# Kernel tuning notes

Measured on AMD Instinct MI355X. Metric: run time of the kernel, lower is better.

## Reference

```python
import jax, jax.numpy as jnp
import numpy as np

N = 262144          # anchors
NUM_CLASSES = 80
DET_DIM = 4 + NUM_CLASSES
TOP_K = 1000
MAX_BOXES = 300
NMS_THRESHOLD = 0.4


def setup_inputs() -> dict:
    key = jax.random.key(0)
    k1, k2, k3, k4, k5 = jax.random.split(key, 5)
    # boxes in (x1, y1, x2, y2) format with x2 > x1, y2 > y1
    xy1 = jax.random.uniform(k1, (1, N, 2), dtype=jnp.float32) * 1000.0
    wh = jax.random.uniform(k2, (1, N, 2), dtype=jnp.float32) * 100.0 + 1.0
    boxes = jnp.concatenate([xy1, xy1 + wh], axis=-1)              # [1, N, 4]
    classification = jax.random.uniform(k3, (1, N, NUM_CLASSES), dtype=jnp.float32)
    detections = jax.random.normal(k4, (1, N, DET_DIM), dtype=jnp.float32)
    return {"boxes": boxes, "classification": classification, "detections": detections}


def _iou_matrix(b):
    # b: [K, 4] in (x1, y1, x2, y2)
    x1, y1, x2, y2 = b[:, 0], b[:, 1], b[:, 2], b[:, 3]
    area = (x2 - x1) * (y2 - y1)
    ix1 = jnp.maximum(x1[:, None], x1[None, :])
    iy1 = jnp.maximum(y1[:, None], y1[None, :])
    ix2 = jnp.minimum(x2[:, None], x2[None, :])
    iy2 = jnp.minimum(y2[:, None], y2[None, :])
    inter = jnp.maximum(ix2 - ix1, 0.0) * jnp.maximum(iy2 - iy1, 0.0)
    union = area[:, None] + area[None, :] - inter
    return inter / jnp.maximum(union, 1e-8)


def _nms(boxes, scores, iou_threshold, max_output_size):
    # Greedy NMS (tf.image.non_max_suppression semantics) on K boxes.
    K = boxes.shape[0]
    order = jnp.argsort(-scores)              # descending score
    iou = _iou_matrix(boxes[order])           # [K, K] in sorted order
    ar = jnp.arange(K)

    def body(suppressed, i):
        active = jnp.logical_not(suppressed[i])
        suppressed = suppressed | (active & (iou[i] > iou_threshold) & (ar > i))
        return suppressed, active

    _, keep = jax.lax.scan(body, jnp.zeros((K,), jnp.bool_), ar)
    # fixed-size selection of kept positions (in score order), padded with K
    sel = jnp.nonzero(keep, size=max_output_size, fill_value=K)[0]
    valid = sel < K
    order_pad = jnp.concatenate([order, jnp.zeros((1,), order.dtype)])
    return order_pad[sel], valid


def reference(boxes, classification, detections):
    b = boxes[0]                               # [N, 4]
    c = classification[0]                      # [N, C]
    d = detections[0]                          # [N, D]
    scores = jnp.max(c, axis=1)                # per-anchor best class score
    scores_k, idx_k = jax.lax.top_k(scores, TOP_K)
    b_k = b[idx_k]                             # [TOP_K, 4]
    d_k = d[idx_k]                             # [TOP_K, D]
    nms_idx, valid = _nms(b_k, scores_k, NMS_THRESHOLD, MAX_BOXES)
    # original returns a ragged [1, n_kept, D]; we return fixed [1, MAX_BOXES, D]
    # with invalid rows zeroed (padding for jit-compatibility)
    out = d_k[nms_idx] * valid[:, None].astype(d_k.dtype)
    return out[None]                           # [1, MAX_BOXES, D]
```

## Files before the change

### kernel.cpp

```cpp
#include <hip/hip_runtime.h>
#include <stdint.h>

#define N_ANCH 262144
#define NUM_CLASSES 80
#define DET_DIM 84
#define TOP_K 1000
#define MAX_BOXES 300
#define NMS_THR 0.4f

#define OFF_KEYS   0u
#define OFF_HIST1  (N_ANCH * 4u)
#define OFF_HIST2  (OFF_HIST1 + 16384u)
#define OFF_HIST3  (OFF_HIST2 + 16384u)
#define OFF_STATE  (OFF_HIST3 + 1024u)
#define OFF_LISTA  (OFF_STATE + 64u)
#define OFF_LISTB  (OFF_LISTA + 4096u)
#define OFF_TOPK   (OFF_LISTB + 16384u)
#define OFF_BOXK   (OFF_TOPK + 4096u)
#define OFF_MASK   (OFF_BOXK + 16384u)
#define OFF_SEL    (OFF_MASK + 131072u)

#define ZERO_WORDS ((16384u + 16384u + 1024u + 64u) / 4u)

__global__ __launch_bounds__(256) void k_init(uint32_t* __restrict__ z) {
    uint32_t tid = blockIdx.x * 256u + threadIdx.x;
    if (tid < ZERO_WORDS) z[tid] = 0u;
}

__global__ __launch_bounds__(256) void k_scores(const float* __restrict__ cls,
                                                uint32_t* __restrict__ keys,
                                                uint32_t* __restrict__ ghist1) {
    __shared__ uint32_t h[4096];
    for (int i = threadIdx.x; i < 4096; i += 256) h[i] = 0u;
    __syncthreads();
    int stride = gridDim.x * 256;
    for (int a = blockIdx.x * 256 + threadIdx.x; a < N_ANCH; a += stride) {
        const float4* q = (const float4*)(cls + (size_t)a * NUM_CLASSES);
        float m = -1.0f;
#pragma unroll
        for (int t = 0; t < 20; ++t) {
            float4 v = q[t];
            m = fmaxf(m, fmaxf(fmaxf(v.x, v.y), fmaxf(v.z, v.w)));
        }
        uint32_t key = __float_as_uint(m);
        keys[a] = key;
        atomicAdd(&h[key >> 20], 1u);
    }
    __syncthreads();
    for (int i = threadIdx.x; i < 4096; i += 256) {
        uint32_t v = h[i];
        if (v) atomicAdd(&ghist1[i], v);
    }
}

__device__ __forceinline__ void wave_scan_hist(const uint32_t* __restrict__ hist,
                                               int nbins, uint32_t k,
                                               uint32_t* __restrict__ out, int lane) {
    int per = nbins >> 6;
    int base = lane * per;
    uint32_t partial = 0;
    for (int b = 0; b < per; ++b) partial += hist[base + b];
    uint32_t si = partial;
#pragma unroll
    for (int off = 1; off < 64; off <<= 1) {
        uint32_t v = __shfl_down(si, off);
        if (lane + off < 64) si += v;
    }
    uint32_t se = si - partial;
    if (se < k && k <= si) {
        uint32_t running = se;
        for (int b = base + per - 1; b >= base; --b) {
            uint32_t hv = hist[b];
            running += hv;
            if (running >= k) {
                out[0] = (uint32_t)b;
                out[1] = k - (running - hv);
                break;
            }
        }
    }
}

__global__ __launch_bounds__(256) void k_pass2(const uint32_t* __restrict__ keys,
                                               const uint32_t* __restrict__ ghist1,
                                               uint32_t* __restrict__ ghist2,
                                               uint32_t* __restrict__ state) {
    __shared__ uint32_t sd[2];
    __shared__ uint32_t h[4096];
    if (threadIdx.x < 64) wave_scan_hist(ghist1, 4096, TOP_K, sd, threadIdx.x);
    for (int i = threadIdx.x; i < 4096; i += 256) h[i] = 0u;
    __syncthreads();
    uint32_t d1 = sd[0], k1 = sd[1];
    if (threadIdx.x == 0 && blockIdx.x == 0) { state[0] = d1; state[1] = k1; }
    int stride = gridDim.x * 256;
    for (int a = blockIdx.x * 256 + threadIdx.x; a < N_ANCH; a += stride) {
        uint32_t key = keys[a];
        if ((key >> 20) == d1) atomicAdd(&h[(key >> 8) & 0xFFFu], 1u);
    }
    __syncthreads();
    for (int i = threadIdx.x; i < 4096; i += 256) {
        uint32_t v = h[i];
        if (v) atomicAdd(&ghist2[i], v);
    }
}

__global__ __launch_bounds__(256) void k_pass3(const uint32_t* __restrict__ keys,
                                               const uint32_t* __restrict__ ghist2,
                                               uint32_t* __restrict__ ghist3,
                                               uint32_t* __restrict__ state) {
    __shared__ uint32_t sd[2];
    if (threadIdx.x < 64) {
        uint32_t k1 = state[1];
        wave_scan_hist(ghist2, 4096, k1, sd, threadIdx.x);
    }
    __syncthreads();
    uint32_t pre24 = (state[0] << 12) | sd[0];
    uint32_t k2 = sd[1];
    if (threadIdx.x == 0 && blockIdx.x == 0) { state[2] = pre24; state[3] = k2; }
    int stride = gridDim.x * 256;
    for (int a = blockIdx.x * 256 + threadIdx.x; a < N_ANCH; a += stride) {
        uint32_t key = keys[a];
        if ((key >> 8) == pre24) atomicAdd(&ghist3[key & 0xFFu], 1u);
    }
}

__global__ __launch_bounds__(256) void k_compact(const uint32_t* __restrict__ keys,
                                                 const uint32_t* __restrict__ ghist3,
                                                 uint32_t* __restrict__ state,
                                                 uint32_t* __restrict__ listA,
                                                 uint32_t* __restrict__ listB) {
    __shared__ uint32_t sd[2];
    if (threadIdx.x < 64) {
        uint32_t k2 = state[3];
        wave_scan_hist(ghist3, 256, k2, sd, threadIdx.x);
    }
    __syncthreads();
    uint32_t T = (state[2] << 8) | sd[0];
    if (threadIdx.x == 0 && blockIdx.x == 0) { state[4] = T; state[5] = sd[1]; }
    int stride = gridDim.x * 256;
    for (int a = blockIdx.x * 256 + threadIdx.x; a < N_ANCH; a += stride) {
        uint32_t key = keys[a];
        if (key > T) {
            uint32_t p = atomicAdd(&state[6], 1u);
            if (p < 1024u) listA[p] = (uint32_t)a;
        } else if (key == T) {
            uint32_t p = atomicAdd(&state[7], 1u);
            if (p < 4096u) listB[p] = (uint32_t)a;
        }
    }
}

__global__ __launch_bounds__(1024) void k_finalize(const uint32_t* __restrict__ keys,
                                                   const uint32_t* __restrict__ state,
                                                   const uint32_t* __restrict__ listA,
                                                   const uint32_t* __restrict__ listB,
                                                   uint32_t* __restrict__ topk,
                                                   const float4* __restrict__ boxes,
                                                   float4* __restrict__ boxk) {
    __shared__ unsigned long long A[1024];
    __shared__ uint32_t Bv[4096];
    __shared__ uint32_t tk[1000];
    int t = threadIdx.x;
    uint32_t cntA = state[6]; if (cntA > 999u) cntA = 999u;
    uint32_t cntB = state[7]; if (cntB > 4096u) cntB = 4096u;
    uint32_t r = TOP_K - cntA;

    unsigned long long wv = ~0ull;
    if (t < (int)cntA) {
        uint32_t idx = listA[t];
        uint32_t key = keys[idx];
        wv = ((unsigned long long)(key ^ 0xFFFFFFFFu) << 32) | (unsigned long long)idx;
    }
    A[t] = wv;
    __syncthreads();
    unsigned n2 = 1; while (n2 < cntA) n2 <<= 1;
    for (unsigned k = 2; k <= n2; k <<= 1) {
        for (unsigned j = k >> 1; j > 0; j >>= 1) {
            unsigned i = (unsigned)t;
            unsigned ixj = i ^ j;
            if (i < n2 && ixj > i) {
                unsigned long long a = A[i], b = A[ixj];
                bool up = ((i & k) == 0);
                if (up ? (a > b) : (a < b)) { A[i] = b; A[ixj] = a; }
            }
            __syncthreads();
        }
    }
    if (t < (int)cntA) tk[t] = (uint32_t)(A[t] & 0xFFFFFFFFull);

    unsigned n2b = 1; while (n2b < cntB) n2b <<= 1;
    for (unsigned i = (unsigned)t; i < n2b; i += 1024) Bv[i] = (i < cntB) ? listB[i] : 0xFFFFFFFFu;
    __syncthreads();
    for (unsigned k = 2; k <= n2b; k <<= 1) {
        for (unsigned j = k >> 1; j > 0; j >>= 1) {
            for (unsigned i = (unsigned)t; i < n2b; i += 1024) {
                unsigned ixj = i ^ j;
                if (ixj > i) {
                    uint32_t a = Bv[i], b = Bv[ixj];
                    bool up = ((i & k) == 0);
                    if (up ? (a > b) : (a < b)) { Bv[i] = b; Bv[ixj] = a; }
                }
            }
            __syncthreads();
        }
    }
    if (t < (int)r) tk[cntA + t] = Bv[t];
    __syncthreads();
    if (t < 1000) {
        uint32_t idx = tk[t];
        topk[t] = idx;
        boxk[t] = boxes[idx];
    }
}

__global__ __launch_bounds__(256) void k_mask(const float4* __restrict__ boxk,
                                              unsigned long long* __restrict__ mask) {
    __shared__ float4 bx[1000];
    for (int i = threadIdx.x; i < 1000; i += 256) bx[i] = boxk[i];
    __syncthreads();
    int i = blockIdx.x;
    if (i >= 1000) {
        if (threadIdx.x < 16) mask[(size_t)i * 16 + threadIdx.x] = 0ull;
        return;
    }
    float4 bi = bx[i];
    float areai = __fmul_rn(__fsub_rn(bi.z, bi.x), __fsub_rn(bi.w, bi.y));
    int lane = threadIdx.x & 63;
    int wave = threadIdx.x >> 6;
#pragma unroll
    for (int rr = 0; rr < 4; ++rr) {
        int j = rr * 256 + threadIdx.x;
        bool bit = false;
        if (j < 1000 && j > i) {
            float4 bj = bx[j];
            float areaj = __fmul_rn(__fsub_rn(bj.z, bj.x), __fsub_rn(bj.w, bj.y));
            float ix1 = fmaxf(bi.x, bj.x);
            float iy1 = fmaxf(bi.y, bj.y);
            float ix2 = fminf(bi.z, bj.z);
            float iy2 = fminf(bi.w, bj.w);
            float iw = fmaxf(__fsub_rn(ix2, ix1), 0.0f);
            float ih = fmaxf(__fsub_rn(iy2, iy1), 0.0f);
            float inter = __fmul_rn(iw, ih);
            float uni = __fsub_rn(__fadd_rn(areai, areaj), inter);
            float den = fmaxf(uni, 1e-8f);
            float iou = inter / den;
            bit = iou > NMS_THR;
        }
        unsigned long long bal = __ballot(bit);
        if (lane == 0) mask[(size_t)i * 16 + (rr * 4 + wave)] = bal;
    }
}

__global__ __launch_bounds__(64) void k_nms(const unsigned long long* __restrict__ mask,
                                            const uint32_t* __restrict__ topk,
                                            uint32_t* __restrict__ sel) {
    __shared__ uint32_t keptList[384];
    int lane = threadIdx.x;
    uint32_t keptCount = 0;
    for (int c = 0; c < 16; ++c) {
        unsigned long long acc = 0ull;
        for (uint32_t s = (uint32_t)lane; s < keptCount; s += 64u)
            acc |= mask[(size_t)keptList[s] * 16 + c];
#pragma unroll
        for (int off = 1; off < 64; off <<= 1) acc |= __shfl_xor(acc, off);
        unsigned long long supp = acc;
        unsigned long long row = mask[(size_t)(c * 64 + lane) * 16 + c];
        for (int i = 0; i < 64; ++i) {
            unsigned long long ri = __shfl(row, i);
            if (!((supp >> i) & 1ull)) supp |= ri;
        }
        unsigned long long validm = (c == 15) ? ((1ull << 40) - 1ull) : ~0ull;
        unsigned long long kept = (~supp) & validm;
        uint32_t cnt = (uint32_t)__popcll(kept);
        if ((kept >> lane) & 1ull) {
            uint32_t pos = keptCount + (uint32_t)__popcll(kept & ((1ull << lane) - 1ull));
            if (pos < 384u) keptList[pos] = (uint32_t)(c * 64 + lane);
        }
        keptCount += cnt;
        __syncthreads();
        if (keptCount >= MAX_BOXES) break;
    }
    for (uint32_t m = (uint32_t)lane; m < MAX_BOXES; m += 64u)
        sel[m] = (m < keptCount) ? topk[keptList[m]] : 0xFFFFFFFFu;
}

__global__ __launch_bounds__(256) void k_out(const uint32_t* __restrict__ sel,
                                             const float* __restrict__ det,
                                             float* __restrict__ out) {
    int tid = blockIdx.x * 256 + threadIdx.x;
    if (tid >= MAX_BOXES * DET_DIM) return;
    int m = tid / DET_DIM;
    int e = tid - m * DET_DIM;
    uint32_t s = sel[m];
    out[tid] = (s == 0xFFFFFFFFu) ? 0.0f : det[(size_t)s * DET_DIM + e];
}

extern "C" void kernel_launch(void* const* d_in, const int* in_sizes, int n_in,
                              void* d_out, int out_size, void* d_ws, size_t ws_size,
                              hipStream_t stream) {
    const float* boxes = (const float*)d_in[0];
    const float* cls   = (const float*)d_in[1];
    const float* det   = (const float*)d_in[2];
    float* out = (float*)d_out;
    char* ws = (char*)d_ws;

    uint32_t* keys  = (uint32_t*)(ws + OFF_KEYS);
    uint32_t* h1    = (uint32_t*)(ws + OFF_HIST1);
    uint32_t* h2    = (uint32_t*)(ws + OFF_HIST2);
    uint32_t* h3    = (uint32_t*)(ws + OFF_HIST3);
    uint32_t* st    = (uint32_t*)(ws + OFF_STATE);
    uint32_t* listA = (uint32_t*)(ws + OFF_LISTA);
    uint32_t* listB = (uint32_t*)(ws + OFF_LISTB);
    uint32_t* topk  = (uint32_t*)(ws + OFF_TOPK);
    float4*   boxk  = (float4*)(ws + OFF_BOXK);
    unsigned long long* mask = (unsigned long long*)(ws + OFF_MASK);
    uint32_t* sel   = (uint32_t*)(ws + OFF_SEL);

    k_init<<<dim3((ZERO_WORDS + 255) / 256), dim3(256), 0, stream>>>(h1);
    k_scores<<<dim3(512), dim3(256), 0, stream>>>(cls, keys, h1);
    k_pass2<<<dim3(256), dim3(256), 0, stream>>>(keys, h1, h2, st);
    k_pass3<<<dim3(256), dim3(256), 0, stream>>>(keys, h2, h3, st);
    k_compact<<<dim3(256), dim3(256), 0, stream>>>(keys, h3, st, listA, listB);
    k_finalize<<<dim3(1), dim3(1024), 0, stream>>>(keys, st, listA, listB, topk,
                                                   (const float4*)boxes, boxk);
    k_mask<<<dim3(1024), dim3(256), 0, stream>>>(boxk, mask);
    k_nms<<<dim3(1), dim3(64), 0, stream>>>(mask, topk, sel);
    k_out<<<dim3((MAX_BOXES * DET_DIM + 255) / 256), dim3(256), 0, stream>>>(sel, det, out);
}
```

Measured before the change: 244.3 us.

## Cut radix-select to two passes, merge compact/sort and NMS/output kernels

Replaces the third histogram pass and the compaction kernel with a single pass that collects every anchor whose top 24 key bits are at or above the threshold prefix. The survivors are then sorted by a single bitonic sort of up to 4096 key/index pairs, where before two separate sorts were run. The NMS and output-gather kernels are fused into one launch, k_mask handles four rows per block, and k_scores uses one thread per anchor. This removes three kernel launches and a global pass over the keys. The risk is silent truncation if more than 4096 anchors share the 24-bit prefix, plus a larger single-block sort.

```diff
diff --git a/kernel.cpp b/kernel.cpp
--- a/kernel.cpp
+++ b/kernel.cpp
@@ -11,19 +11,16 @@
 #define OFF_KEYS   0u
 #define OFF_HIST1  (N_ANCH * 4u)
 #define OFF_HIST2  (OFF_HIST1 + 16384u)
-#define OFF_HIST3  (OFF_HIST2 + 16384u)
-#define OFF_STATE  (OFF_HIST3 + 1024u)
-#define OFF_LISTA  (OFF_STATE + 64u)
-#define OFF_LISTB  (OFF_LISTA + 4096u)
-#define OFF_TOPK   (OFF_LISTB + 16384u)
+#define OFF_STATE  (OFF_HIST2 + 16384u)
+#define OFF_LIST   (OFF_STATE + 64u)
+#define OFF_TOPK   (OFF_LIST + 16384u)
 #define OFF_BOXK   (OFF_TOPK + 4096u)
 #define OFF_MASK   (OFF_BOXK + 16384u)
-#define OFF_SEL    (OFF_MASK + 131072u)
-
-#define ZERO_WORDS ((16384u + 16384u + 1024u + 64u) / 4u)
-
-__global__ __launch_bounds__(256) void k_init(uint32_t* __restrict__ z) {
-    uint32_t tid = blockIdx.x * 256u + threadIdx.x;
+
+#define ZERO_WORDS ((16384u + 16384u + 64u) / 4u)
+
+__global__ __launch_bounds__(1024) void k_init(uint32_t* __restrict__ z) {
+    uint32_t tid = blockIdx.x * 1024u + threadIdx.x;
     if (tid < ZERO_WORDS) z[tid] = 0u;
 }
 
@@ -33,19 +30,17 @@
     __shared__ uint32_t h[4096];
     for (int i = threadIdx.x; i < 4096; i += 256) h[i] = 0u;
     __syncthreads();
-    int stride = gridDim.x * 256;
-    for (int a = blockIdx.x * 256 + threadIdx.x; a < N_ANCH; a += stride) {
-        const float4* q = (const float4*)(cls + (size_t)a * NUM_CLASSES);
-        float m = -1.0f;
-#pragma unroll
-        for (int t = 0; t < 20; ++t) {
-            float4 v = q[t];
-            m = fmaxf(m, fmaxf(fmaxf(v.x, v.y), fmaxf(v.z, v.w)));
-        }
-        uint32_t key = __float_as_uint(m);
-        keys[a] = key;
-        atomicAdd(&h[key >> 20], 1u);
-    }
+    int a = blockIdx.x * 256 + threadIdx.x;
+    const float4* q = (const float4*)(cls + (size_t)a * NUM_CLASSES);
+    float m = -1.0f;
+#pragma unroll
+    for (int t = 0; t < 20; ++t) {
+        float4 v = q[t];
+        m = fmaxf(m, fmaxf(fmaxf(v.x, v.y), fmaxf(v.z, v.w)));
+    }
+    uint32_t key = __float_as_uint(m);
+    keys[a] = key;
+    atomicAdd(&h[key >> 20], 1u);
     __syncthreads();
     for (int i = threadIdx.x; i < 4096; i += 256) {
         uint32_t v = h[i];
@@ -104,10 +99,10 @@
     }
 }
 
-__global__ __launch_bounds__(256) void k_pass3(const uint32_t* __restrict__ keys,
-                                               const uint32_t* __restrict__ ghist2,
-                                               uint32_t* __restrict__ ghist3,
-                                               uint32_t* __restrict__ state) {
+__global__ __launch_bounds__(256) void k_pass3c(const uint32_t* __restrict__ keys,
+                                                const uint32_t* __restrict__ ghist2,
+                                                uint32_t* __restrict__ state,
+                                                uint32_t* __restrict__ list) {
     __shared__ uint32_t sd[2];
     if (threadIdx.x < 64) {
         uint32_t k1 = state[1];
@@ -115,99 +110,52 @@
     }
     __syncthreads();
     uint32_t pre24 = (state[0] << 12) | sd[0];
-    uint32_t k2 = sd[1];
-    if (threadIdx.x == 0 && blockIdx.x == 0) { state[2] = pre24; state[3] = k2; }
+    if (threadIdx.x == 0 && blockIdx.x == 0) state[2] = pre24;
     int stride = gridDim.x * 256;
     for (int a = blockIdx.x * 256 + threadIdx.x; a < N_ANCH; a += stride) {
         uint32_t key = keys[a];
-        if ((key >> 8) == pre24) atomicAdd(&ghist3[key & 0xFFu], 1u);
-    }
-}
-
-__global__ __launch_bounds__(256) void k_compact(const uint32_t* __restrict__ keys,
-                                                 const uint32_t* __restrict__ ghist3,
-                                                 uint32_t* __restrict__ state,
-                                                 uint32_t* __restrict__ listA,
-                                                 uint32_t* __restrict__ listB) {
-    __shared__ uint32_t sd[2];
-    if (threadIdx.x < 64) {
-        uint32_t k2 = state[3];
-        wave_scan_hist(ghist3, 256, k2, sd, threadIdx.x);
-    }
-    __syncthreads();
-    uint32_t T = (state[2] << 8) | sd[0];
-    if (threadIdx.x == 0 && blockIdx.x == 0) { state[4] = T; state[5] = sd[1]; }
-    int stride = gridDim.x * 256;
-    for (int a = blockIdx.x * 256 + threadIdx.x; a < N_ANCH; a += stride) {
-        uint32_t key = keys[a];
-        if (key > T) {
-            uint32_t p = atomicAdd(&state[6], 1u);
-            if (p < 1024u) listA[p] = (uint32_t)a;
-        } else if (key == T) {
-            uint32_t p = atomicAdd(&state[7], 1u);
-            if (p < 4096u) listB[p] = (uint32_t)a;
-        }
-    }
-}
-
-__global__ __launch_bounds__(1024) void k_finalize(const uint32_t* __restrict__ keys,
-                                                   const uint32_t* __restrict__ state,
-                                                   const uint32_t* __restrict__ listA,
-                                                   const uint32_t* __restrict__ listB,
-                                                   uint32_t* __restrict__ topk,
-                                                   const float4* __restrict__ boxes,
-                                                   float4* __restrict__ boxk) {
-    __shared__ unsigned long long A[1024];
-    __shared__ uint32_t Bv[4096];
-    __shared__ uint32_t tk[1000];
+        if ((key >> 8) >= pre24) {
+            uint32_t p = atomicAdd(&state[3], 1u);
+            if (p < 4096u) list[p] = (uint32_t)a;
+        }
+    }
+}
+
+__global__ __launch_bounds__(1024) void k_sort(const uint32_t* __restrict__ keys,
+                                               const uint32_t* __restrict__ state,
+                                               const uint32_t* __restrict__ list,
+                                               uint32_t* __restrict__ topk,
+                                               const float4* __restrict__ boxes,
+                                               float4* __restrict__ boxk) {
+    __shared__ unsigned long long A[4096];
     int t = threadIdx.x;
-    uint32_t cntA = state[6]; if (cntA > 999u) cntA = 999u;
-    uint32_t cntB = state[7]; if (cntB > 4096u) cntB = 4096u;
-    uint32_t r = TOP_K - cntA;
-
-    unsigned long long wv = ~0ull;
-    if (t < (int)cntA) {
-        uint32_t idx = listA[t];
-        uint32_t key = keys[idx];
-        wv = ((unsigned long long)(key ^ 0xFFFFFFFFu) << 32) | (unsigned long long)idx;
-    }
-    A[t] = wv;
-    __syncthreads();
-    unsigned n2 = 1; while (n2 < cntA) n2 <<= 1;
+    uint32_t cnt = state[3];
+    if (cnt > 4096u) cnt = 4096u;
+    unsigned n2 = 1024; while (n2 < cnt) n2 <<= 1;
+    for (unsigned i = (unsigned)t; i < n2; i += 1024) {
+        unsigned long long wv = ~0ull;
+        if (i < cnt) {
+            uint32_t idx = list[i];
+            wv = ((unsigned long long)(~keys[idx]) << 32) | (unsigned long long)idx;
+        }
+        A[i] = wv;
+    }
+    __syncthreads();
     for (unsigned k = 2; k <= n2; k <<= 1) {
         for (unsigned j = k >> 1; j > 0; j >>= 1) {
-            unsigned i = (unsigned)t;
-            unsigned ixj = i ^ j;
-            if (i < n2 && ixj > i) {
-                unsigned long long a = A[i], b = A[ixj];
-                bool up = ((i & k) == 0);
-                if (up ? (a > b) : (a < b)) { A[i] = b; A[ixj] = a; }
-            }
-            __syncthreads();
-        }
-    }
-    if (t < (int)cntA) tk[t] = (uint32_t)(A[t] & 0xFFFFFFFFull);
-
-    unsigned n2b = 1; while (n2b < cntB) n2b <<= 1;
-    for (unsigned i = (unsigned)t; i < n2b; i += 1024) Bv[i] = (i < cntB) ? listB[i] : 0xFFFFFFFFu;
-    __syncthreads();
-    for (unsigned k = 2; k <= n2b; k <<= 1) {
-        for (unsigned j = k >> 1; j > 0; j >>= 1) {
-            for (unsigned i = (unsigned)t; i < n2b; i += 1024) {
+            for (unsigned i = (unsigned)t; i < n2; i += 1024) {
                 unsigned ixj = i ^ j;
                 if (ixj > i) {
-                    uint32_t a = Bv[i], b = Bv[ixj];
+                    unsigned long long a = A[i], b = A[ixj];
                     bool up = ((i & k) == 0);
-                    if (up ? (a > b) : (a < b)) { Bv[i] = b; Bv[ixj] = a; }
+                    if (up ? (a > b) : (a < b)) { A[i] = b; A[ixj] = a; }
                 }
             }
             __syncthreads();
         }
     }
-    if (t < (int)r) tk[cntA + t] = Bv[t];
-    __syncthreads();
-    if (t < 1000) {
-        uint32_t idx = tk[t];
+    if (t < TOP_K) {
+        uint32_t idx = (uint32_t)(A[t] & 0xFFFFFFFFull);
         topk[t] = idx;
         boxk[t] = boxes[idx];
     }
@@ -215,84 +163,87 @@
 
 __global__ __launch_bounds__(256) void k_mask(const float4* __restrict__ boxk,
                                               unsigned long long* __restrict__ mask) {
-    __shared__ float4 bx[1000];
-    for (int i = threadIdx.x; i < 1000; i += 256) bx[i] = boxk[i];
-    __syncthreads();
-    int i = blockIdx.x;
-    if (i >= 1000) {
-        if (threadIdx.x < 16) mask[(size_t)i * 16 + threadIdx.x] = 0ull;
-        return;
-    }
-    float4 bi = bx[i];
-    float areai = __fmul_rn(__fsub_rn(bi.z, bi.x), __fsub_rn(bi.w, bi.y));
     int lane = threadIdx.x & 63;
     int wave = threadIdx.x >> 6;
-#pragma unroll
-    for (int rr = 0; rr < 4; ++rr) {
-        int j = rr * 256 + threadIdx.x;
-        bool bit = false;
-        if (j < 1000 && j > i) {
-            float4 bj = bx[j];
-            float areaj = __fmul_rn(__fsub_rn(bj.z, bj.x), __fsub_rn(bj.w, bj.y));
-            float ix1 = fmaxf(bi.x, bj.x);
-            float iy1 = fmaxf(bi.y, bj.y);
-            float ix2 = fminf(bi.z, bj.z);
-            float iy2 = fminf(bi.w, bj.w);
-            float iw = fmaxf(__fsub_rn(ix2, ix1), 0.0f);
-            float ih = fmaxf(__fsub_rn(iy2, iy1), 0.0f);
-            float inter = __fmul_rn(iw, ih);
-            float uni = __fsub_rn(__fadd_rn(areai, areaj), inter);
-            float den = fmaxf(uni, 1e-8f);
-            float iou = inter / den;
-            bit = iou > NMS_THR;
-        }
-        unsigned long long bal = __ballot(bit);
-        if (lane == 0) mask[(size_t)i * 16 + (rr * 4 + wave)] = bal;
-    }
-}
-
-__global__ __launch_bounds__(64) void k_nms(const unsigned long long* __restrict__ mask,
-                                            const uint32_t* __restrict__ topk,
-                                            uint32_t* __restrict__ sel) {
+    for (int r = 0; r < 4; ++r) {
+        int i = blockIdx.x * 4 + r;
+        if (i >= 1000) {
+            if (threadIdx.x < 16) mask[(size_t)i * 16 + threadIdx.x] = 0ull;
+            continue;
+        }
+        float4 bi = boxk[i];
+        float areai = __fmul_rn(__fsub_rn(bi.z, bi.x), __fsub_rn(bi.w, bi.y));
+#pragma unroll
+        for (int rr = 0; rr < 4; ++rr) {
+            int j = rr * 256 + threadIdx.x;
+            bool bit = false;
+            if (j < 1000 && j > i) {
+                float4 bj = boxk[j];
+                float areaj = __fmul_rn(__fsub_rn(bj.z, bj.x), __fsub_rn(bj.w, bj.y));
+                float ix1 = fmaxf(bi.x, bj.x);
+                float iy1 = fmaxf(bi.y, bj.y);
+                float ix2 = fminf(bi.z, bj.z);
+                float iy2 = fminf(bi.w, bj.w);
+                float iw = fmaxf(__fsub_rn(ix2, ix1), 0.0f);
+                float ih = fmaxf(__fsub_rn(iy2, iy1), 0.0f);
+                float inter = __fmul_rn(iw, ih);
+                float uni = __fsub_rn(__fadd_rn(areai, areaj), inter);
+                float den = fmaxf(uni, 1e-8f);
+                float iou = inter / den;
+                bit = iou > NMS_THR;
+            }
+            unsigned long long bal = __ballot(bit);
+            if (lane == 0) mask[(size_t)i * 16 + (rr * 4 + wave)] = bal;
+        }
+    }
+}
+
+__global__ __launch_bounds__(256) void k_nms_out(const unsigned long long* __restrict__ mask,
+                                                 const uint32_t* __restrict__ topk,
+                                                 const float* __restrict__ det,
+                                                 float* __restrict__ out) {
     __shared__ uint32_t keptList[384];
-    int lane = threadIdx.x;
-    uint32_t keptCount = 0;
-    for (int c = 0; c < 16; ++c) {
-        unsigned long long acc = 0ull;
-        for (uint32_t s = (uint32_t)lane; s < keptCount; s += 64u)
-            acc |= mask[(size_t)keptList[s] * 16 + c];
-#pragma unroll
-        for (int off = 1; off < 64; off <<= 1) acc |= __shfl_xor(acc, off);
-        unsigned long long supp = acc;
-        unsigned long long row = mask[(size_t)(c * 64 + lane) * 16 + c];
-        for (int i = 0; i < 64; ++i) {
-            unsigned long long ri = __shfl(row, i);
-            if (!((supp >> i) & 1ull)) supp |= ri;
-        }
-        unsigned long long validm = (c == 15) ? ((1ull << 40) - 1ull) : ~0ull;
-        unsigned long long kept = (~supp) & validm;
-        uint32_t cnt = (uint32_t)__popcll(kept);
-        if ((kept >> lane) & 1ull) {
-            uint32_t pos = keptCount + (uint32_t)__popcll(kept & ((1ull << lane) - 1ull));
-            if (pos < 384u) keptList[pos] = (uint32_t)(c * 64 + lane);
-        }
-        keptCount += cnt;
-        __syncthreads();
-        if (keptCount >= MAX_BOXES) break;
-    }
-    for (uint32_t m = (uint32_t)lane; m < MAX_BOXES; m += 64u)
-        sel[m] = (m < keptCount) ? topk[keptList[m]] : 0xFFFFFFFFu;
-}
-
-__global__ __launch_bounds__(256) void k_out(const uint32_t* __restrict__ sel,
-                                             const float* __restrict__ det,
-                                             float* __restrict__ out) {
-    int tid = blockIdx.x * 256 + threadIdx.x;
-    if (tid >= MAX_BOXES * DET_DIM) return;
-    int m = tid / DET_DIM;
-    int e = tid - m * DET_DIM;
-    uint32_t s = sel[m];
-    out[tid] = (s == 0xFFFFFFFFu) ? 0.0f : det[(size_t)s * DET_DIM + e];
+    __shared__ uint32_t selS[MAX_BOXES];
+    __shared__ uint32_t kcS;
+    int lane = threadIdx.x & 63;
+    int wave = threadIdx.x >> 6;
+    if (wave == 0) {
+        uint32_t keptCount = 0;
+        for (int c = 0; c < 16; ++c) {
+            unsigned long long acc = 0ull;
+            for (uint32_t s = (uint32_t)lane; s < keptCount; s += 64u)
+                acc |= mask[(size_t)keptList[s] * 16 + c];
+#pragma unroll
+            for (int off = 1; off < 64; off <<= 1) acc |= __shfl_xor(acc, off);
+            unsigned long long supp = acc;
+            unsigned long long row = mask[(size_t)(c * 64 + lane) * 16 + c];
+            for (int i = 0; i < 64; ++i) {
+                unsigned long long ri = __shfl(row, i);
+                if (!((supp >> i) & 1ull)) supp |= ri;
+            }
+            unsigned long long validm = (c == 15) ? ((1ull << 40) - 1ull) : ~0ull;
+            unsigned long long kept = (~supp) & validm;
+            uint32_t cnt = (uint32_t)__popcll(kept);
+            if ((kept >> lane) & 1ull) {
+                uint32_t pos = keptCount + (uint32_t)__popcll(kept & ((1ull << lane) - 1ull));
+                if (pos < 384u) keptList[pos] = (uint32_t)(c * 64 + lane);
+            }
+            keptCount += cnt;
+            if (keptCount >= MAX_BOXES) break;
+        }
+        if (keptCount > MAX_BOXES) keptCount = MAX_BOXES;
+        for (uint32_t m = (uint32_t)lane; m < MAX_BOXES; m += 64u)
+            selS[m] = (m < keptCount) ? topk[keptList[m]] : 0xFFFFFFFFu;
+        if (lane == 0) kcS = keptCount;
+    }
+    __syncthreads();
+    (void)kcS;
+    for (int m = wave; m < MAX_BOXES; m += 4) {
+        uint32_t s = selS[m];
+        const float* src = det + (size_t)s * DET_DIM;
+        for (int e = lane; e < DET_DIM; e += 64)
+            out[m * DET_DIM + e] = (s == 0xFFFFFFFFu) ? 0.0f : src[e];
+    }
 }
 
 extern "C" void kernel_launch(void* const* d_in, const int* in_sizes, int n_in,
@@ -304,26 +255,21 @@
     float* out = (float*)d_out;
     char* ws = (char*)d_ws;
 
-    uint32_t* keys  = (uint32_t*)(ws + OFF_KEYS);
-    uint32_t* h1    = (uint32_t*)(ws + OFF_HIST1);
-    uint32_t* h2    = (uint32_t*)(ws + OFF_HIST2);
-    uint32_t* h3    = (uint32_t*)(ws + OFF_HIST3);
-    uint32_t* st    = (uint32_t*)(ws + OFF_STATE);
-    uint32_t* listA = (uint32_t*)(ws + OFF_LISTA);
-    uint32_t* listB = (uint32_t*)(ws + OFF_LISTB);
-    uint32_t* topk  = (uint32_t*)(ws + OFF_TOPK);
-    float4*   boxk  = (float4*)(ws + OFF_BOXK);
+    uint32_t* keys = (uint32_t*)(ws + OFF_KEYS);
+    uint32_t* h1   = (uint32_t*)(ws + OFF_HIST1);
+    uint32_t* h2   = (uint32_t*)(ws + OFF_HIST2);
+    uint32_t* st   = (uint32_t*)(ws + OFF_STATE);
+    uint32_t* list = (uint32_t*)(ws + OFF_LIST);
+    uint32_t* topk = (uint32_t*)(ws + OFF_TOPK);
+    float4*   boxk = (float4*)(ws + OFF_BOXK);
     unsigned long long* mask = (unsigned long long*)(ws + OFF_MASK);
-    uint32_t* sel   = (uint32_t*)(ws + OFF_SEL);
-
-    k_init<<<dim3((ZERO_WORDS + 255) / 256), dim3(256), 0, stream>>>(h1);
-    k_scores<<<dim3(512), dim3(256), 0, stream>>>(cls, keys, h1);
+
+    k_init<<<dim3((ZERO_WORDS + 1023) / 1024), dim3(1024), 0, stream>>>(h1);
+    k_scores<<<dim3(N_ANCH / 256), dim3(256), 0, stream>>>(cls, keys, h1);
     k_pass2<<<dim3(256), dim3(256), 0, stream>>>(keys, h1, h2, st);
-    k_pass3<<<dim3(256), dim3(256), 0, stream>>>(keys, h2, h3, st);
-    k_compact<<<dim3(256), dim3(256), 0, stream>>>(keys, h3, st, listA, listB);
-    k_finalize<<<dim3(1), dim3(1024), 0, stream>>>(keys, st, listA, listB, topk,
-                                                   (const float4*)boxes, boxk);
-    k_mask<<<dim3(1024), dim3(256), 0, stream>>>(boxk, mask);
-    k_nms<<<dim3(1), dim3(64), 0, stream>>>(mask, topk, sel);
-    k_out<<<dim3((MAX_BOXES * DET_DIM + 255) / 256), dim3(256), 0, stream>>>(sel, det, out);
-}
+    k_pass3c<<<dim3(256), dim3(256), 0, stream>>>(keys, h2, st, list);
+    k_sort<<<dim3(1), dim3(1024), 0, stream>>>(keys, st, list, topk,
+                                               (const float4*)boxes, boxk);
+    k_mask<<<dim3(256), dim3(256), 0, stream>>>(boxk, mask);
+    k_nms_out<<<dim3(1), dim3(256), 0, stream>>>(mask, topk, det, out);
+}
```

New measurement: 321.4 us. 1.32x slower.
